# Kernel optimization log

Measured on AMD Instinct MI355X. Metric: run time of the kernel, lower is better.

Reference implementation:

```python
import jax, jax.numpy as jnp
import numpy as np

ENT = 16
INNER = 64
NEG = 1e12

def _rope_sin_cos(seq_len, dim, dtype):
    # interleaved sinusoidal: pos_emb[s] = [sin0, cos0, sin1, cos1, ...]
    pos = jnp.arange(seq_len, dtype=jnp.float32)[:, None]          # [S,1]
    freqs = jnp.power(10000.0, -2.0 * jnp.arange(dim // 2, dtype=jnp.float32) / dim)
    ang = pos * freqs                                              # [S,D/2]
    sin = jnp.repeat(jnp.sin(ang), 2, axis=-1).astype(dtype)       # [S,D] (each value doubled)
    cos = jnp.repeat(jnp.cos(ang), 2, axis=-1).astype(dtype)       # [S,D]
    return sin[None, :, None, :], cos[None, :, None, :]            # broadcast to [B,S,E,D]

def _rotate_half_interleaved(x):
    # stack([-x[...,1::2], x[...,0::2]], -1).reshape(x.shape)
    return jnp.stack([-x[..., 1::2], x[..., 0::2]], axis=-1).reshape(x.shape)

def setup_inputs() -> dict:
    key = jax.random.key(0)
    k1, k2 = jax.random.split(key)
    B, S, H = 4, 1024, 1024
    last_hidden_state = jax.random.normal(k1, (B, S, H), dtype=jnp.float32)
    W_dense = jax.random.normal(k2, (H, ENT * INNER * 2), dtype=jnp.float32) * (1.0 / np.sqrt(H))
    b_dense = jnp.zeros((ENT * INNER * 2,), dtype=jnp.float32)
    token_lengh = jnp.ones((B, S), dtype=jnp.float32)  # 0/1 padding mask over key positions
    return {"last_hidden_state": last_hidden_state, "W_dense": W_dense,
            "b_dense": b_dense, "token_lengh": token_lengh}

def reference(last_hidden_state, W_dense, b_dense, token_lengh):
    B, S, H = last_hidden_state.shape
    # dense -> [B,S,E,2D]; split into q,k heads per entity type
    out = (last_hidden_state @ W_dense + b_dense).reshape(B, S, ENT, 2 * INNER)
    qw, kw = out[..., :INNER], out[..., INNER:]
    # inline RoPE
    sin, cos = _rope_sin_cos(S, INNER, qw.dtype)
    qw = qw * cos + _rotate_half_interleaved(qw) * sin
    kw = kw * cos + _rotate_half_interleaved(kw) * sin
    # pairwise biaffine scores per entity type
    logits = jnp.einsum('bmhd,bnhd->bhmn', qw, kw)                 # [B,E,S,S]
    # padding mask (key dim only, matching the torch expand semantics)
    pad = token_lengh[:, None, None, :]                            # [B,1,1,S]
    logits = logits * pad - (1.0 - pad) * NEG
    # strict lower-triangular mask (spans with end < start are invalid)
    tril = jnp.tril(jnp.ones((S, S), dtype=logits.dtype), -1)
    logits = logits - tril * NEG
    return logits / jnp.sqrt(jnp.asarray(INNER, dtype=logits.dtype))
```

## Files before the change

### kernel.cpp

```cpp
#include <hip/hip_runtime.h>
#include <hip/hip_bf16.h>
#include <stdint.h>

#define B_   4
#define S_   1024
#define H_   1024
#define NH_  16
#define D_   64
#define N1_  2048
#define M1_  4096
#define NEG_ 1000000000000.0f

typedef __attribute__((ext_vector_type(8))) short bf16x8;
typedef __attribute__((ext_vector_type(4))) float f32x4;

__device__ inline void gload_lds16(const void* g, void* l) {
  __builtin_amdgcn_global_load_lds(
      (const __attribute__((address_space(1))) unsigned int*)g,
      (__attribute__((address_space(3))) unsigned int*)l, 16, 0, 0);
}

__device__ inline unsigned short f2bf(float f) {
  union { float f; uint32_t u; } a; a.f = f;
  uint32_t r = a.u + 0x7fff + ((a.u >> 16) & 1);
  return (unsigned short)(r >> 16);
}


__global__ __launch_bounds__(256) void k_prep(
    const float4* __restrict__ lhs4, unsigned short* __restrict__ lhsb,
    const float* __restrict__ W, unsigned short* __restrict__ WT,
    float* __restrict__ tab) {
  __shared__ float tsm[32][33];
  int b = blockIdx.x, t = threadIdx.x;
  if (b < 4096) {
    int i = b * 256 + t;
    float4 v = lhs4[i];
    uint64_t pk = (uint64_t)f2bf(v.x) | ((uint64_t)f2bf(v.y) << 16) |
                  ((uint64_t)f2bf(v.z) << 32) | ((uint64_t)f2bf(v.w) << 48);
    ((uint64_t*)lhsb)[i] = pk;
  } else if (b < 6144) {
    int bb = b - 4096;
    int nb = (bb & 63) * 32, kb = (bb >> 6) * 32;
    int tx = t & 31, ty = t >> 5;
    for (int r = 0; r < 4; r++)
      tsm[ty + r * 8][tx] = W[(size_t)(kb + ty + r * 8) * N1_ + nb + tx];
    __syncthreads();
    for (int r = 0; r < 4; r++)
      WT[(size_t)(nb + ty + r * 8) * H_ + kb + tx] = f2bf(tsm[tx][ty + r * 8]);
  } else {
    int i = (b - 6144) * 256 + t;
    int pos = i >> 5, fi = i & 31;
    float freq = exp2f(-(float)fi * (13.2877123795494f / 32.0f));
    float ang = (float)pos * freq;
    tab[2 * i]     = sinf(ang);
    tab[2 * i + 1] = cosf(ang);
  }
}


__global__ __launch_bounds__(256) void k_gemm1(
    const unsigned short* __restrict__ A,
    const unsigned short* __restrict__ BT,
    const float* __restrict__ bias,
    const float* __restrict__ sc,
    unsigned short* __restrict__ qws,
    unsigned short* __restrict__ kws) {
  __shared__ unsigned short a_lds[128 * 32];
  __shared__ unsigned short b_lds[128 * 32];
  int t = threadIdx.x;
  int lane = t & 63, wv = t >> 6;
  int wm = wv >> 1, wn = wv & 1;
  int col = lane & 15, quad = lane >> 4;

  int l = blockIdx.x;
  int xcd = l & 7, k = l >> 3;
  int mBase = (((k & 3) << 3) + xcd) * 128;
  int nBase = (k >> 2) * 128;

  f32x4 acc[4][4] = {};

  for (int kk = 0; kk < H_; kk += 32) {
    for (int c = 0; c < 2; c++) {
      int idx = c * 256 + t;
      int r = idx >> 2, ch = idx & 3;
      gload_lds16(A + (size_t)(mBase + r) * H_ + kk + ch * 8, a_lds + idx * 8);
      gload_lds16(BT + (size_t)(nBase + r) * H_ + kk + ch * 8, b_lds + idx * 8);
    }
    __syncthreads();
    bf16x8 af[4], bf[4];
#pragma unroll
    for (int i = 0; i < 4; i++)
      af[i] = *(const bf16x8*)&a_lds[(wm * 64 + i * 16 + col) * 32 + quad * 8];
#pragma unroll
    for (int j = 0; j < 4; j++)
      bf[j] = *(const bf16x8*)&b_lds[(wn * 64 + j * 16 + col) * 32 + quad * 8];
#pragma unroll
    for (int j = 0; j < 4; j++)
#pragma unroll
      for (int i = 0; i < 4; i++)
        acc[j][i] = __builtin_amdgcn_mfma_f32_16x16x32_bf16(bf[j], af[i], acc[j][i], 0, 0, 0);
    __syncthreads();
  }

#pragma unroll
  for (int i = 0; i < 4; i++) {
    int m = mBase + wm * 64 + i * 16 + col;
    int pos = m & (S_ - 1);
    int bb = m >> 10;
#pragma unroll
    for (int j = 0; j < 4; j++) {
      int n = nBase + wn * 64 + j * 16 + quad * 4;
      int d = n & 63;
      int head = n >> 7;
      int isK = (n >> 6) & 1;
      float4 bj  = *(const float4*)&bias[n];
      float4 scv = *(const float4*)&sc[(pos * 32 + (d >> 1)) * 2];
      float v0 = acc[j][i][0] + bj.x;
      float v1 = acc[j][i][1] + bj.y;
      float v2 = acc[j][i][2] + bj.z;
      float v3 = acc[j][i][3] + bj.w;
      float o0 = v0 * scv.y - v1 * scv.x;
      float o1 = v1 * scv.y + v0 * scv.x;
      float o2 = v2 * scv.w - v3 * scv.z;
      float o3 = v3 * scv.w + v2 * scv.z;
      unsigned short* dst = isK ? kws : qws;
      ushort4 pk;
      pk.x = f2bf(o0); pk.y = f2bf(o1); pk.z = f2bf(o2); pk.w = f2bf(o3);
      *(ushort4*)&dst[((size_t)(bb * NH_ + head) * S_ + pos) * D_ + d] = pk;
    }
  }
}


#define STG_ 132

__global__ __launch_bounds__(256) void k_gemm2(
    const unsigned short* __restrict__ qws,
    const unsigned short* __restrict__ kws,
    const float* __restrict__ tl,
    float* __restrict__ out) {
  __shared__ __align__(16) char smem[64 * STG_ * 4];
  unsigned short* q_lds = (unsigned short*)smem;
  unsigned short* k_lds = q_lds + 128 * 64;
  float* stage = (float*)smem;

  int t = threadIdx.x;
  int lane = t & 63, wv = t >> 6, wm = wv >> 1, wn = wv & 1;
  int col = lane & 15, quad = lane >> 4;

  int l = blockIdx.x;
  int xcd = l & 7, k = l >> 3;
  int z = (xcd << 3) + (k >> 6);
  int tile = k & 63;
  int mt = tile >> 3, nt = tile & 7;
  int mT = mt * 128, nT = nt * 128;
  int bb = z >> 4;

  if (nt < mt) {
    int c4 = (t & 31) * 4;
    int r0 = t >> 5;
    int n = nT + c4;
    float4 pad4 = *(const float4*)&tl[bb * S_ + n];
    f32x4 o;
    o.x = (-(1.0f - pad4.x) * NEG_ - NEG_) * 0.125f;
    o.y = (-(1.0f - pad4.y) * NEG_ - NEG_) * 0.125f;
    o.z = (-(1.0f - pad4.z) * NEG_ - NEG_) * 0.125f;
    o.w = (-(1.0f - pad4.w) * NEG_ - NEG_) * 0.125f;
#pragma unroll
    for (int r = 0; r < 16; r++) {
      int m = mT + r * 8 + r0;
      __builtin_nontemporal_store(o, (f32x4*)&out[((size_t)z * S_ + m) * S_ + n]);
    }
    return;
  }

  const unsigned short* qb = qws + ((size_t)z * S_ + mT) * D_;
  const unsigned short* kb = kws + ((size_t)z * S_ + nT) * D_;

  for (int c = 0; c < 4; c++) {
    int idx = c * 256 + t;
    gload_lds16(qb + idx * 8, q_lds + idx * 8);
    gload_lds16(kb + idx * 8, k_lds + idx * 8);
  }
  __syncthreads();

  f32x4 acc[4][4] = {};
#pragma unroll
  for (int kk = 0; kk < 64; kk += 32) {
    bf16x8 qf[4], kf[4];
#pragma unroll
    for (int i = 0; i < 4; i++)
      qf[i] = *(const bf16x8*)&q_lds[(wm * 64 + i * 16 + col) * 64 + kk + quad * 8];
#pragma unroll
    for (int j = 0; j < 4; j++)
      kf[j] = *(const bf16x8*)&k_lds[(wn * 64 + j * 16 + col) * 64 + kk + quad * 8];
#pragma unroll
    for (int j = 0; j < 4; j++)
#pragma unroll
      for (int i = 0; i < 4; i++)
        acc[j][i] = __builtin_amdgcn_mfma_f32_16x16x32_bf16(kf[j], qf[i], acc[j][i], 0, 0, 0);
  }
  __syncthreads();

#pragma unroll
  for (int half = 0; half < 2; half++) {
    if (wm == half) {
#pragma unroll
      for (int i = 0; i < 4; i++) {
        int rloc = i * 16 + col;
#pragma unroll
        for (int j = 0; j < 4; j++) {
          int cloc = wn * 64 + j * 16 + quad * 4;
          float4 v;
          v.x = acc[j][i][0]; v.y = acc[j][i][1];
          v.z = acc[j][i][2]; v.w = acc[j][i][3];
          *(float4*)&stage[rloc * STG_ + cloc] = v;
        }
      }
    }
    __syncthreads();
    int mbase = mT + half * 64;
#pragma unroll
    for (int r = 0; r < 8; r++) {
      int f = r * 256 + t;
      int rloc = f >> 5;
      int c4 = (f & 31) * 4;
      float4 v = *(const float4*)&stage[rloc * STG_ + c4];
      int m = mbase + rloc;
      int n = nT + c4;
      float4 pad4 = *(const float4*)&tl[bb * S_ + n];
      f32x4 o;
      float x;
      x = v.x * pad4.x - (1.0f - pad4.x) * NEG_; if (m > n)     x -= NEG_; o.x = x * 0.125f;
      x = v.y * pad4.y - (1.0f - pad4.y) * NEG_; if (m > n + 1) x -= NEG_; o.y = x * 0.125f;
      x = v.z * pad4.z - (1.0f - pad4.z) * NEG_; if (m > n + 2) x -= NEG_; o.z = x * 0.125f;
      x = v.w * pad4.w - (1.0f - pad4.w) * NEG_; if (m > n + 3) x -= NEG_; o.w = x * 0.125f;
      __builtin_nontemporal_store(o, (f32x4*)&out[((size_t)z * S_ + m) * S_ + n]);
    }
    __syncthreads();
  }
}


extern "C" void kernel_launch(void* const* d_in, const int* in_sizes, int n_in,
                              void* d_out, int out_size, void* d_ws, size_t ws_size,
                              hipStream_t stream) {
  const float* lhs  = (const float*)d_in[0];
  const float* W    = (const float*)d_in[1];
  const float* bias = (const float*)d_in[2];
  const float* tl   = (const float*)d_in[3];
  float* out = (float*)d_out;

  char* ws = (char*)d_ws;
  unsigned short* lhsb = (unsigned short*)(ws);
  unsigned short* WT   = (unsigned short*)(ws + (8u  << 20));
  unsigned short* qws  = (unsigned short*)(ws + (12u << 20));
  unsigned short* kws  = (unsigned short*)(ws + (20u << 20));
  float*          sc   = (float*)        (ws + (28u << 20));

  k_prep<<<6272, 256, 0, stream>>>((const float4*)lhs, lhsb, W, WT, sc);
  k_gemm1<<<512, 256, 0, stream>>>(lhsb, WT, bias, sc, qws, kws);
  k_gemm2<<<4096, 256, 0, stream>>>(qws, kws, tl, out);
}
```

Measured before the change: 318.3 us.

## Double-buffer GEMM1 LDS tiles and XOR-swizzle to avoid bank conflicts

The projection GEMM kernel now keeps two LDS buffers. It issues the global-to-LDS loads for the next K slice before computing on the current one, so memory latency can overlap with MFMA work and one barrier per iteration is dropped. The LDS layout also XOR-swizzles the 16-byte chunk index by row, which is meant to reduce bank conflicts on fragment reads. In exchange the kernel uses twice as much LDS, which may lower occupancy.

```diff
diff --git a/kernel.cpp b/kernel.cpp
--- a/kernel.cpp
+++ b/kernel.cpp
@@ -66,41 +66,59 @@
     const float* __restrict__ sc,
     unsigned short* __restrict__ qws,
     unsigned short* __restrict__ kws) {
-  __shared__ unsigned short a_lds[128 * 32];
-  __shared__ unsigned short b_lds[128 * 32];
+  __shared__ unsigned short a_lds[2][128 * 32];
+  __shared__ unsigned short b_lds[2][128 * 32];
   int t = threadIdx.x;
   int lane = t & 63, wv = t >> 6;
   int wm = wv >> 1, wn = wv & 1;
   int col = lane & 15, quad = lane >> 4;
+  int swz8 = (quad ^ ((col >> 1) & 3)) * 8;
 
   int l = blockIdx.x;
   int xcd = l & 7, k = l >> 3;
   int mBase = (((k & 3) << 3) + xcd) * 128;
   int nBase = (k >> 2) * 128;
 
+  int idx0 = t;
+  int idx1 = 256 + t;
+  int r0 = idx0 >> 2, ch0 = (idx0 & 3) ^ ((r0 >> 1) & 3);
+  int r1 = idx1 >> 2, ch1 = (idx1 & 3) ^ ((r1 >> 1) & 3);
+  const unsigned short* Arow0 = A + (size_t)(mBase + r0) * H_ + ch0 * 8;
+  const unsigned short* Arow1 = A + (size_t)(mBase + r1) * H_ + ch1 * 8;
+  const unsigned short* Brow0 = BT + (size_t)(nBase + r0) * H_ + ch0 * 8;
+  const unsigned short* Brow1 = BT + (size_t)(nBase + r1) * H_ + ch1 * 8;
+
   f32x4 acc[4][4] = {};
 
+  gload_lds16(Arow0, &a_lds[0][idx0 * 8]);
+  gload_lds16(Brow0, &b_lds[0][idx0 * 8]);
+  gload_lds16(Arow1, &a_lds[0][idx1 * 8]);
+  gload_lds16(Brow1, &b_lds[0][idx1 * 8]);
+  __syncthreads();
+
+  int p = 0;
   for (int kk = 0; kk < H_; kk += 32) {
-    for (int c = 0; c < 2; c++) {
-      int idx = c * 256 + t;
-      int r = idx >> 2, ch = idx & 3;
-      gload_lds16(A + (size_t)(mBase + r) * H_ + kk + ch * 8, a_lds + idx * 8);
-      gload_lds16(BT + (size_t)(nBase + r) * H_ + kk + ch * 8, b_lds + idx * 8);
-    }
-    __syncthreads();
+    if (kk + 32 < H_) {
+      int q = p ^ 1;
+      gload_lds16(Arow0 + kk + 32, &a_lds[q][idx0 * 8]);
+      gload_lds16(Brow0 + kk + 32, &b_lds[q][idx0 * 8]);
+      gload_lds16(Arow1 + kk + 32, &a_lds[q][idx1 * 8]);
+      gload_lds16(Brow1 + kk + 32, &b_lds[q][idx1 * 8]);
+    }
     bf16x8 af[4], bf[4];
 #pragma unroll
     for (int i = 0; i < 4; i++)
-      af[i] = *(const bf16x8*)&a_lds[(wm * 64 + i * 16 + col) * 32 + quad * 8];
-#pragma unroll
-    for (int j = 0; j < 4; j++)
-      bf[j] = *(const bf16x8*)&b_lds[(wn * 64 + j * 16 + col) * 32 + quad * 8];
+      af[i] = *(const bf16x8*)&a_lds[p][(wm * 64 + i * 16 + col) * 32 + swz8];
+#pragma unroll
+    for (int j = 0; j < 4; j++)
+      bf[j] = *(const bf16x8*)&b_lds[p][(wn * 64 + j * 16 + col) * 32 + swz8];
 #pragma unroll
     for (int j = 0; j < 4; j++)
 #pragma unroll
       for (int i = 0; i < 4; i++)
         acc[j][i] = __builtin_amdgcn_mfma_f32_16x16x32_bf16(bf[j], af[i], acc[j][i], 0, 0, 0);
     __syncthreads();
+    p ^= 1;
   }
 
 #pragma unroll
```

After: 314.3 us (median of 2 runs). Within noise of the previous version (-1.2%).
